# Kernel tuning notes

Measured on AMD Instinct MI355X. Metric: run time of the kernel, lower is better.

The kernel has to match this reference:

```python
import jax, jax.numpy as jnp
import numpy as np

EPS = 1e-6          # module eps for denominator
KERNEL_EPS = 1e-4   # performer softmax_kernel numerical eps


def softmax_kernel(data, projection):
    # data: [n, l, h, e]; projection: [m, e] -> features [n, l, h, m]
    d = data.shape[-1]
    m = projection.shape[0]
    data_normalizer = d ** -0.25
    ratio = m ** -0.5
    data_dash = jnp.einsum('nlhe,me->nlhm', data * data_normalizer, projection)
    diag_data = (0.5 * (data_normalizer ** 2)) * jnp.sum(data * data, axis=-1, keepdims=True)
    # numerically stable exp with per-row max subtraction
    data_dash = ratio * (jnp.exp(data_dash - diag_data - jnp.max(data_dash, axis=-1, keepdims=True)) + KERNEL_EPS)
    return data_dash


def _gaussian_orthogonal_random_matrix(nb_rows, nb_cols, seed=0):
    rng = np.random.default_rng(seed)
    blocks = []
    for _ in range(int(np.ceil(nb_rows / nb_cols))):
        q, _ = np.linalg.qr(rng.standard_normal((nb_cols, nb_cols)))
        blocks.append(q.T)
    proj = np.concatenate(blocks, axis=0)[:nb_rows]
    # scaling=0: chi-distributed row multipliers
    multiplier = np.linalg.norm(rng.standard_normal((nb_rows, nb_cols)), axis=1)
    return (multiplier[:, None] * proj).astype(np.float32)


def setup_inputs() -> dict:
    n, l, h, e = 2, 2048, 8, 64
    nb_features = l  # module: nb_features = l when l >= e
    key = jax.random.key(0)
    kq, kk, kv = jax.random.split(key, 3)
    queries = jax.random.normal(kq, (n, l, h, e), jnp.float32)
    keys = jax.random.normal(kk, (n, l, h, e), jnp.float32)
    values = jax.random.normal(kv, (n, l, h, e), jnp.float32)
    projection = jnp.asarray(_gaussian_orthogonal_random_matrix(nb_features, e))
    return {"queries": queries, "keys": keys, "values": values, "projection": projection}


def reference(queries, keys, values, projection):
    # Performer linear attention, batched (bi=None) branch
    q = softmax_kernel(queries, projection)   # [n, l, h, m]
    k = softmax_kernel(keys, projection)      # [n, l, h, m]
    kv = jnp.einsum('nshm,nshe->nhem', k, values)              # [n, h, e, m]
    z = 1.0 / (jnp.einsum('nlhm,nhm->nlh', q, k.sum(axis=1)) + EPS)  # [n, l, h]
    v = jnp.einsum('nlhm,nhem,nlh->nlhe', q, kv, z)             # [n, l, h, e]
    return v
```

## Files before the change

### kernel.cpp

```cpp
#include <hip/hip_runtime.h>


#define LL 2048
#define HH 8
#define MM 2048
#define ROWSTR 512

#define NORMC 0.35355339059327373f
#define RATIO 0.022097086912079608f
#define KEPS 1e-4f
#define REPS (RATIO * KEPS)
#define EPSD 1e-6f

#define KVSPLIT 2097152
#define RSPLIT 32768

typedef __attribute__((ext_vector_type(8))) short short8;
typedef __attribute__((ext_vector_type(16))) float f32x16;

#define MFMA32(a, b, c) __builtin_amdgcn_mfma_f32_32x32x16_bf16((a), (b), (c), 0, 0, 0)

__device__ __forceinline__ f32x16 zero16() {
    f32x16 v;
    #pragma unroll
    for (int i = 0; i < 16; ++i) v[i] = 0.f;
    return v;
}
__device__ __forceinline__ unsigned short f2bf(float f) {
    union { float f; unsigned int u; } v; v.f = f;
    unsigned int r = v.u + 0x7fffu + ((v.u >> 16) & 1u);
    return (unsigned short)(r >> 16);
}
__device__ __forceinline__ unsigned int pk2(float lo, float hi) {
    return __builtin_amdgcn_perm(__float_as_uint(hi), __float_as_uint(lo), 0x07060302u);
}
__device__ __forceinline__ float bf2f(unsigned short u) {
    union { unsigned int ui; float f; } v; v.ui = ((unsigned int)u) << 16; return v.f;
}

template <bool BF16>
__device__ __forceinline__ void tile_load(const void* src, size_t base, size_t rstride,
                                          int t, uint4& A, uint4& B) {
    const int row = t >> 2, c16 = (t & 3) * 16;
    if (BF16) {
        const unsigned short* p = (const unsigned short*)src + base + (size_t)row * rstride + c16;
        A = *(const uint4*)p;
        B = *(const uint4*)(p + 8);
    } else {
        const float* p = (const float*)src + base + (size_t)row * rstride + c16;
        float4 f0 = ((const float4*)p)[0], f1 = ((const float4*)p)[1];
        float4 f2 = ((const float4*)p)[2], f3 = ((const float4*)p)[3];
        A.x = pk2(f0.x, f0.y); A.y = pk2(f0.z, f0.w);
        A.z = pk2(f1.x, f1.y); A.w = pk2(f1.z, f1.w);
        B.x = pk2(f2.x, f2.y); B.y = pk2(f2.z, f2.w);
        B.z = pk2(f3.x, f3.y); B.w = pk2(f3.z, f3.w);
    }
}
__device__ __forceinline__ void tile_store72(unsigned short* D, int t, uint4 A, uint4 B) {
    const int row = t >> 2, c16 = (t & 3) * 16;
    *(uint4*)&D[row * 72 + c16] = A;
    *(uint4*)&D[row * 72 + c16 + 8] = B;
}

template <bool BF16>
__device__ __forceinline__ void vt_load(const void* V, size_t base, int t, uint4& A, uint4& B) {
    const int s0 = (t & 31) * 2, e0 = (t >> 5) * 8;
    if (BF16) {
        const unsigned short* p = (const unsigned short*)V + base + (size_t)s0 * ROWSTR + e0;
        A = *(const uint4*)p;
        B = *(const uint4*)(p + ROWSTR);
    } else {
        const float* p = (const float*)V + base + (size_t)s0 * ROWSTR + e0;
        float4 f0 = ((const float4*)p)[0], f1 = ((const float4*)p)[1];
        const float* q = p + ROWSTR;
        float4 g0 = ((const float4*)q)[0], g1 = ((const float4*)q)[1];
        A.x = pk2(f0.x, f0.y); A.y = pk2(f0.z, f0.w);
        A.z = pk2(f1.x, f1.y); A.w = pk2(f1.z, f1.w);
        B.x = pk2(g0.x, g0.y); B.y = pk2(g0.z, g0.w);
        B.z = pk2(g1.x, g1.y); B.w = pk2(g1.z, g1.w);
    }
}
__device__ __forceinline__ void vt_store72(unsigned short* VT, int t, uint4 A, uint4 B) {
    const int s0 = (t & 31) * 2, e0 = (t >> 5) * 8;
    const unsigned ua[4] = {A.x, A.y, A.z, A.w}, ub[4] = {B.x, B.y, B.z, B.w};
    #pragma unroll
    for (int i = 0; i < 4; ++i) {
        *(unsigned*)&VT[(e0 + 2 * i) * 72 + s0] = (ua[i] & 0xFFFFu) | (ub[i] << 16);
        *(unsigned*)&VT[(e0 + 2 * i + 1) * 72 + s0] = (ua[i] >> 16) | (ub[i] & 0xFFFF0000u);
    }
}

__device__ __forceinline__ short8 xfrag(const unsigned int pd[8], int cp, int hi) {
    const unsigned int s0 = hi ? pd[4 * cp + 0] : pd[4 * cp + 2];
    const unsigned int s1 = hi ? pd[4 * cp + 1] : pd[4 * cp + 3];
    const unsigned int r0 = (unsigned int)__shfl_xor((int)s0, 32);
    const unsigned int r1 = (unsigned int)__shfl_xor((int)s1, 32);
    union { unsigned int u[4]; short8 s; } v;
    v.u[0] = hi ? r0 : pd[4 * cp + 0];
    v.u[1] = hi ? r1 : pd[4 * cp + 1];
    v.u[2] = hi ? pd[4 * cp + 2] : r0;
    v.u[3] = hi ? pd[4 * cp + 3] : r1;
    return v.s;
}

__global__ void LinearAttention_15985868276494_detect(const unsigned short* __restrict__ P,
                                                      float* __restrict__ flag) {
    if (threadIdx.x == 0) {
        int sane = 1;
        #pragma unroll
        for (int i = 0; i < 16; ++i) {
            const unsigned e = (P[2 * i] >> 7) & 0xFF;
            if (e < 101 || e > 141) sane = 0;
        }
        *flag = sane ? 1.0f : 0.0f;
    }
}

template <bool BF16>
__device__ void stats_impl(const void* X, const void* P, float* cws,
                           unsigned short* Xs, unsigned short* Ps, float* red) {
    const int t = threadIdx.x;
    const int w = t >> 6, ln = t & 31, hi = (t >> 5) & 1;
    const int row_base = blockIdx.x * 128;

    uint4 a0, b0, a1, b1;
    tile_load<BF16>(X, (size_t)row_base * 64, 64, t, a0, b0);
    tile_store72(Xs, t, a0, b0);
    tile_load<BF16>(X, (size_t)(row_base + 64) * 64, 64, t, a1, b1);
    tile_store72(Xs + 64 * 72, t, a1, b1);
    tile_load<BF16>(P, 0, 64, t, a0, b0);
    tile_store72(Ps, t, a0, b0);
    tile_load<BF16>(P, (size_t)64 * 64, 64, t, a1, b1);
    tile_store72(Ps + 64 * 72, t, a1, b1);
    uint4 pA0, pB0, pA1, pB1;
    tile_load<BF16>(P, (size_t)128 * 64, 64, t, pA0, pB0);
    tile_load<BF16>(P, (size_t)192 * 64, 64, t, pA1, pB1);
    __syncthreads();

    short8 xb[4][4];
    #pragma unroll
    for (int xs = 0; xs < 4; ++xs)
        #pragma unroll
        for (int c = 0; c < 4; ++c)
            xb[xs][c] = *(const short8*)&Xs[(32 * xs + ln) * 72 + 16 * c + 8 * hi];

    float rmax4[4] = {-3e38f, -3e38f, -3e38f, -3e38f};
    for (int mt = 0; mt < 16; ++mt) {
        const int cur = mt & 1;
        unsigned short* Pc = Ps + cur * (128 * 72);
        if (mt + 1 < 16) {
            unsigned short* Pn = Ps + (cur ^ 1) * (128 * 72);
            tile_store72(Pn, t, pA0, pB0);
            tile_store72(Pn + 64 * 72, t, pA1, pB1);
            if (mt + 2 < 16) {
                tile_load<BF16>(P, (size_t)((mt + 2) * 128) * 64, 64, t, pA0, pB0);
                tile_load<BF16>(P, (size_t)((mt + 2) * 128 + 64) * 64, 64, t, pA1, pB1);
            }
        }
        #pragma unroll
        for (int xs = 0; xs < 4; ++xs) {
            f32x16 acc = zero16();
            #pragma unroll
            for (int c = 0; c < 4; ++c) {
                const short8 af = *(const short8*)&Pc[(32 * w + ln) * 72 + 16 * c + 8 * hi];
                acc = MFMA32(af, xb[xs][c], acc);
            }
            float m = acc[0];
            #pragma unroll
            for (int r = 1; r < 16; ++r) m = fmaxf(m, acc[r]);
            rmax4[xs] = fmaxf(rmax4[xs], m);
        }
        __syncthreads();
    }
    #pragma unroll
    for (int xs = 0; xs < 4; ++xs) {
        const float m = fmaxf(rmax4[xs], __shfl_xor(rmax4[xs], 32));
        if (hi == 0) red[w * 128 + xs * 32 + ln] = m;
    }
    __syncthreads();
    if (t < 128) {
        const float rm = fmaxf(fmaxf(red[t], red[128 + t]), fmaxf(red[256 + t], red[384 + t]));
        float s2 = 0.f;
        #pragma unroll
        for (int c = 0; c < 64; c += 8) {
            uint4 u = *(const uint4*)&Xs[t * 72 + c];
            const unsigned int ua[4] = {u.x, u.y, u.z, u.w};
            #pragma unroll
            for (int i = 0; i < 4; ++i) {
                const float lo = bf2f((unsigned short)(ua[i] & 0xFFFF));
                const float hv = bf2f((unsigned short)(ua[i] >> 16));
                s2 = fmaf(lo, lo, s2); s2 = fmaf(hv, hv, s2);
            }
        }
        const int rg = row_base + t;
        const int n = rg >> 14, l = (rg >> 3) & 2047, h = rg & 7;
        cws[(size_t)((n << 3) | h) * LL + l] = NORMC * rm + (0.5f * NORMC * NORMC) * s2;
    }
}

__global__ __launch_bounds__(256, 2) void LinearAttention_15985868276494_stats(
        const void* K, const void* Q, const void* P, const float* flag,
        float* c_k, float* c_q) {
    __shared__ unsigned short Xs[128 * 72];
    __shared__ unsigned short Ps[2 * 128 * 72];
    __shared__ float red[512];
    const void* X = (blockIdx.y == 0) ? K : Q;
    float* cws = (blockIdx.y == 0) ? c_k : c_q;
    if (*flag != 0.f) stats_impl<true>(X, P, cws, Xs, Ps, red);
    else stats_impl<false>(X, P, cws, Xs, Ps, red);
}

template <bool BF16>
__device__ void kv_impl(const void* K, const void* V, const void* P, const float* cws,
                        float* kvf01, float* ksum01, char* smem) {
    unsigned short* Ks = (unsigned short*)smem;
    unsigned short* VT = (unsigned short*)(smem + 18432);
    unsigned short* Ps = (unsigned short*)(smem + 36864);
    float* cks = (float*)(smem + 46080);
    float* fin = (float*)smem;

    const int t = threadIdx.x;
    const int w = t >> 6, ln = t & 31, hi = (t >> 5) & 1;
    const int sstrip = w & 1, mstrip = w >> 1;
    const int mt = blockIdx.x, nh = blockIdx.y, sp = blockIdx.z;
    const int n = nh >> 3, h = nh & 7;
    const size_t xbase = (size_t)n * (LL * ROWSTR) + (size_t)h * 64;
    const int st0 = sp * 16;

    {
        uint4 pa, pbv;
        tile_load<BF16>(P, (size_t)(mt * 64) * 64, 64, t, pa, pbv);
        tile_store72(Ps, t, pa, pbv);
    }
    uint4 kA, kB, vA, vB; float ckr = 0.f;
    tile_load<BF16>(K, xbase + (size_t)(st0 * 64) * ROWSTR, ROWSTR, t, kA, kB);
    vt_load<BF16>(V, xbase + (size_t)(st0 * 64) * ROWSTR, t, vA, vB);
    if (t < 64) ckr = cws[(size_t)nh * LL + st0 * 64 + t];
    tile_store72(Ks, t, kA, kB);
    vt_store72(VT, t, vA, vB);
    if (t < 64) cks[t] = ckr;
    tile_load<BF16>(K, xbase + (size_t)((st0 + 1) * 64) * ROWSTR, ROWSTR, t, kA, kB);
    vt_load<BF16>(V, xbase + (size_t)((st0 + 1) * 64) * ROWSTR, t, vA, vB);
    if (t < 64) ckr = cws[(size_t)nh * LL + (st0 + 1) * 64 + t];
    __syncthreads();

    short8 pb[4];
    #pragma unroll
    for (int c = 0; c < 4; ++c)
        pb[c] = *(const short8*)&Ps[(32 * mstrip + ln) * 72 + 16 * c + 8 * hi];
    const short8 ones = {0x3F80, 0x3F80, 0x3F80, 0x3F80, 0x3F80, 0x3F80, 0x3F80, 0x3F80};

    f32x16 akv0 = zero16(), akv1 = zero16(), aks = zero16();

    for (int i = 0; i < 16; ++i) {
        const int cur = i & 1;
        unsigned short* Kc = Ks + cur * 4608;
        unsigned short* Vc = VT + cur * 4608;
        const float* cc = cks + cur * 64;
        if (i + 1 < 16) {
            tile_store72(Ks + (cur ^ 1) * 4608, t, kA, kB);
            vt_store72(VT + (cur ^ 1) * 4608, t, vA, vB);
            if (t < 64) cks[(cur ^ 1) * 64 + t] = ckr;
            if (i + 2 < 16) {
                const int st = st0 + i + 2;
                tile_load<BF16>(K, xbase + (size_t)(st * 64) * ROWSTR, ROWSTR, t, kA, kB);
                vt_load<BF16>(V, xbase + (size_t)(st * 64) * ROWSTR, t, vA, vB);
                if (t < 64) ckr = cws[(size_t)nh * LL + st * 64 + t];
            }
        }
        f32x16 D = zero16();
        #pragma unroll
        for (int c = 0; c < 4; ++c) {
            const short8 af = *(const short8*)&Kc[(32 * sstrip + ln) * 72 + 16 * c + 8 * hi];
            D = MFMA32(af, pb[c], D);
        }
        unsigned int pd[8];
        #pragma unroll
        for (int g = 0; g < 4; ++g) {
            const float4 c4 = *(const float4*)&cc[32 * sstrip + 8 * g + 4 * hi];
            const float ca[4] = {c4.x, c4.y, c4.z, c4.w};
            float f[4];
            #pragma unroll
            for (int b = 0; b < 4; ++b) {
                const float arg = fminf(fmaf(D[4 * g + b], NORMC, -ca[b]), 0.f);
                f[b] = fmaf(__expf(arg), RATIO, REPS);
            }
            pd[2 * g] = pk2(f[0], f[1]);
            pd[2 * g + 1] = pk2(f[2], f[3]);
        }
        #pragma unroll
        for (int cp = 0; cp < 2; ++cp) {
            const short8 bf = xfrag(pd, cp, hi);
            const int scol = 32 * sstrip + 16 * cp + 8 * hi;
            const short8 v0 = *(const short8*)&Vc[ln * 72 + scol];
            const short8 v1 = *(const short8*)&Vc[(32 + ln) * 72 + scol];
            akv0 = MFMA32(v0, bf, akv0);
            akv1 = MFMA32(v1, bf, akv1);
            aks = MFMA32(ones, bf, aks);
        }
        __syncthreads();
    }
    {
        const int slot = (w * 64 + (t & 63)) * 36;
        #pragma unroll
        for (int r = 0; r < 16; ++r) fin[slot + r] = akv0[r];
        #pragma unroll
        for (int r = 0; r < 16; ++r) fin[slot + 16 + r] = akv1[r];
        fin[slot + 32] = aks[0];
    }
    __syncthreads();
    {
        const int e = t >> 2;
        const int t16 = e >> 5, e5 = e & 31;
        const int hi_s = (e5 >> 2) & 1;
        const int reg = 16 * t16 + (e5 & 3) + 4 * (e5 >> 3);
        float* dst = kvf01 + (size_t)sp * KVSPLIT + (size_t)nh * (64 * MM)
                   + (size_t)e * MM + mt * 64 + (t & 3) * 16;
        #pragma unroll
        for (int jq = 0; jq < 4; ++jq) {
            float o[4];
            #pragma unroll
            for (int b = 0; b < 4; ++b) {
                const int m_local = (t & 3) * 16 + 4 * jq + b;
                const int ms = m_local >> 5;
                const int lane_s = hi_s * 32 + (m_local & 31);
                o[b] = fin[((2 * ms) * 64 + lane_s) * 36 + reg]
                     + fin[((2 * ms + 1) * 64 + lane_s) * 36 + reg];
            }
            *(float4*)&dst[4 * jq] = make_float4(o[0], o[1], o[2], o[3]);
        }
        if (t < 64) {
            const int ms = t >> 5;
            const float val = fin[((2 * ms) * 64 + (t & 31)) * 36 + 32]
                            + fin[((2 * ms + 1) * 64 + (t & 31)) * 36 + 32];
            ksum01[(size_t)sp * RSPLIT + (size_t)nh * MM + mt * 64 + t] = val;
        }
    }
}

__global__ __launch_bounds__(256, 3) void LinearAttention_15985868276494_kv(
        const void* K, const void* V, const void* P, const float* flag,
        const float* cws, float* kvf01, float* ksum01) {
    extern __shared__ char smem_kv[];
    if (*flag != 0.f) kv_impl<true>(K, V, P, cws, kvf01, ksum01, smem_kv);
    else kv_impl<false>(K, V, P, cws, kvf01, ksum01, smem_kv);
}

__global__ __launch_bounds__(256) void LinearAttention_15985868276494_reduce(
        const float* __restrict__ kvf01, const float* __restrict__ ksum01,
        unsigned short* __restrict__ kvT, float* __restrict__ ksumW) {
    const int gid = blockIdx.x * 256 + threadIdx.x;
    const size_t i4 = (size_t)gid * 4;
    const float4 a = *(const float4*)&kvf01[i4];
    const float4 b = *(const float4*)&kvf01[KVSPLIT + i4];
    uint2 o;
    o.x = (unsigned)f2bf(a.x + b.x) | ((unsigned)f2bf(a.y + b.y) << 16);
    o.y = (unsigned)f2bf(a.z + b.z) | ((unsigned)f2bf(a.w + b.w) << 16);
    *(uint2*)&kvT[i4] = o;
    if (blockIdx.x < 32) {
        const float4 c = *(const float4*)&ksum01[i4];
        const float4 d = *(const float4*)&ksum01[RSPLIT + i4];
        *(float4*)&ksumW[i4] = make_float4(c.x + d.x, c.y + d.y, c.z + d.z, c.w + d.w);
    }
}

template <bool BF16>
__device__ void out_impl(const void* Q, const void* P, const float* cqw,
                         const unsigned short* kvT, const float* ksum, void* outp,
                         char* smem) {
    unsigned short* Qs = (unsigned short*)smem;
    unsigned short* Ps = (unsigned short*)(smem + 9216);
    unsigned short* KVs = (unsigned short*)(smem + 27648);
    unsigned short* kss = (unsigned short*)(smem + 46080);
    float* fin = (float*)(smem + 9216);

    const int t = threadIdx.x;
    const int w = t >> 6, ln = t & 31, hi = (t >> 5) & 1;
    const int mstrip = w & 1, lstrip = w >> 1;
    const int lb = blockIdx.x, nh = blockIdx.y;
    const int n = nh >> 3, h = nh & 7;
    const size_t qbase = (size_t)n * (LL * ROWSTR) + (size_t)h * 64 + (size_t)(lb * 64) * ROWSTR;
    const size_t kvbase = (size_t)nh * (size_t)(64 * MM);

    {
        uint4 qa, qbv;
        tile_load<BF16>(Q, qbase, ROWSTR, t, qa, qbv);
        tile_store72(Qs, t, qa, qbv);
    }
    uint4 pA, pB, kA, kB; float ksr = 0.f;
    tile_load<BF16>(P, 0, 64, t, pA, pB);
    tile_load<true>(kvT, kvbase, MM, t, kA, kB);
    if (t < 64) ksr = ksum[(size_t)nh * MM + t];
    tile_store72(Ps, t, pA, pB);
    tile_store72(KVs, t, kA, kB);
    if (t < 64) kss[t] = f2bf(ksr);
    tile_load<BF16>(P, (size_t)64 * 64, 64, t, pA, pB);
    tile_load<true>(kvT, kvbase + 64, MM, t, kA, kB);
    if (t < 64) ksr = ksum[(size_t)nh * MM + 64 + t];
    __syncthreads();

    short8 qb[4];
    #pragma unroll
    for (int c = 0; c < 4; ++c)
        qb[c] = *(const short8*)&Qs[(32 * lstrip + ln) * 72 + 16 * c + 8 * hi];
    const float cq = cqw[(size_t)nh * LL + lb * 64 + lstrip * 32 + ln];

    f32x16 ao0 = zero16(), ao1 = zero16(), ad = zero16();

    for (int mt = 0; mt < 32; ++mt) {
        const int cur = mt & 1;
        unsigned short* Pc = Ps + cur * 4608;
        unsigned short* Kc = KVs + cur * 4608;
        const unsigned short* ksc = kss + cur * 64;
        if (mt + 1 < 32) {
            tile_store72(Ps + (cur ^ 1) * 4608, t, pA, pB);
            tile_store72(KVs + (cur ^ 1) * 4608, t, kA, kB);
            if (t < 64) kss[(cur ^ 1) * 64 + t] = f2bf(ksr);
            if (mt + 2 < 32) {
                tile_load<BF16>(P, (size_t)((mt + 2) * 64) * 64, 64, t, pA, pB);
                tile_load<true>(kvT, kvbase + (mt + 2) * 64, MM, t, kA, kB);
                if (t < 64) ksr = ksum[(size_t)nh * MM + (mt + 2) * 64 + t];
            }
        }
        f32x16 D = zero16();
        #pragma unroll
        for (int c = 0; c < 4; ++c) {
            const short8 af = *(const short8*)&Pc[(32 * mstrip + ln) * 72 + 16 * c + 8 * hi];
            D = MFMA32(af, qb[c], D);
        }
        unsigned int pd[8];
        #pragma unroll
        for (int g = 0; g < 4; ++g) {
            float f[4];
            #pragma unroll
            for (int b = 0; b < 4; ++b) {
                const float arg = fminf(fmaf(D[4 * g + b], NORMC, -cq), 0.f);
                f[b] = fmaf(__expf(arg), RATIO, REPS);
            }
            pd[2 * g] = pk2(f[0], f[1]);
            pd[2 * g + 1] = pk2(f[2], f[3]);
        }
        #pragma unroll
        for (int cp = 0; cp < 2; ++cp) {
            const short8 bf = xfrag(pd, cp, hi);
            const int mcol = 32 * mstrip + 16 * cp + 8 * hi;
            const short8 a0 = *(const short8*)&Kc[ln * 72 + mcol];
            const short8 a1 = *(const short8*)&Kc[(32 + ln) * 72 + mcol];
            const short8 k8 = *(const short8*)&ksc[mcol];
            ao0 = MFMA32(a0, bf, ao0);
            ao1 = MFMA32(a1, bf, ao1);
            ad = MFMA32(k8, bf, ad);
        }
        __syncthreads();
    }
    {
        const int slot = (w * 64 + (t & 63)) * 36;
        #pragma unroll
        for (int r = 0; r < 16; ++r) fin[slot + r] = ao0[r];
        #pragma unroll
        for (int r = 0; r < 16; ++r) fin[slot + 16 + r] = ao1[r];
        fin[slot + 32] = ad[0];
    }
    __syncthreads();
    {
        const int l_local = t >> 2, eg = t & 3;
        const int ls = l_local >> 5, lane_l = l_local & 31;
        const float adt = fin[((2 * ls) * 64 + lane_l) * 36 + 32]
                        + fin[((2 * ls + 1) * 64 + lane_l) * 36 + 32];
        const float z = 1.0f / (adt + EPSD);
        const int l = lb * 64 + l_local;
        const size_t rowoff = ((size_t)(n * LL + l) * HH + h) * 64 + eg * 16;
        float vals[16];
        #pragma unroll
        for (int j = 0; j < 16; ++j) {
            const int e = eg * 16 + j;
            const int t16 = e >> 5, e5 = e & 31;
            const int hi_s = (e5 >> 2) & 1;
            const int reg = 16 * t16 + (e5 & 3) + 4 * (e5 >> 3);
            const int lane_s = hi_s * 32 + lane_l;
            vals[j] = (fin[((2 * ls) * 64 + lane_s) * 36 + reg]
                     + fin[((2 * ls + 1) * 64 + lane_s) * 36 + reg]) * z;
        }
        if (BF16) {
            uint4 o0, o1;
            o0.x = (unsigned)f2bf(vals[0]) | ((unsigned)f2bf(vals[1]) << 16);
            o0.y = (unsigned)f2bf(vals[2]) | ((unsigned)f2bf(vals[3]) << 16);
            o0.z = (unsigned)f2bf(vals[4]) | ((unsigned)f2bf(vals[5]) << 16);
            o0.w = (unsigned)f2bf(vals[6]) | ((unsigned)f2bf(vals[7]) << 16);
            o1.x = (unsigned)f2bf(vals[8]) | ((unsigned)f2bf(vals[9]) << 16);
            o1.y = (unsigned)f2bf(vals[10]) | ((unsigned)f2bf(vals[11]) << 16);
            o1.z = (unsigned)f2bf(vals[12]) | ((unsigned)f2bf(vals[13]) << 16);
            o1.w = (unsigned)f2bf(vals[14]) | ((unsigned)f2bf(vals[15]) << 16);
            unsigned short* op = (unsigned short*)outp + rowoff;
            *(uint4*)op = o0;
            *(uint4*)(op + 8) = o1;
        } else {
            float* op = (float*)outp + rowoff;
            #pragma unroll
            for (int q4 = 0; q4 < 4; ++q4)
                *(float4*)&op[4 * q4] = make_float4(vals[4 * q4], vals[4 * q4 + 1],
                                                    vals[4 * q4 + 2], vals[4 * q4 + 3]);
        }
    }
}

__global__ __launch_bounds__(256, 3) void LinearAttention_15985868276494_out(
        const void* Q, const void* P, const float* flag, const float* cqw,
        const unsigned short* kvT, const float* ksum, void* outp) {
    extern __shared__ char smem_out[];
    if (*flag != 0.f) out_impl<true>(Q, P, cqw, kvT, ksum, outp, smem_out);
    else out_impl<false>(Q, P, cqw, kvT, ksum, outp, smem_out);
}

extern "C" void kernel_launch(void* const* d_in, const int* in_sizes, int n_in,
                              void* d_out, int out_size, void* d_ws, size_t ws_size,
                              hipStream_t stream) {
    const void* Q = d_in[0];
    const void* K = d_in[1];
    const void* V = d_in[2];
    const void* P = d_in[3];

    float* W = (float*)d_ws;
    float* flag = W;
    float* c_k = W + 16;
    float* c_q = c_k + 32768;
    float* ksum01 = c_q + 32768;
    float* kvf01 = ksum01 + 2 * RSPLIT;
    float* ksumW = kvf01 + 2 * KVSPLIT;
    unsigned short* kvTW = (unsigned short*)(ksumW + RSPLIT);

    LinearAttention_15985868276494_detect<<<1, 64, 0, stream>>>(
        (const unsigned short*)P, flag);
    LinearAttention_15985868276494_stats<<<dim3(256, 2), 256, 0, stream>>>(
        K, Q, P, flag, c_k, c_q);
    LinearAttention_15985868276494_kv<<<dim3(32, 16, 2), 256, 46592, stream>>>(
        K, V, P, flag, c_k, kvf01, ksum01);
    LinearAttention_15985868276494_reduce<<<2048, 256, 0, stream>>>(
        kvf01, ksum01, kvTW, ksumW);
    LinearAttention_15985868276494_out<<<dim3(32, 16), 256, 46592, stream>>>(
        Q, P, flag, c_q, kvTW, ksumW, d_out);
}
```

Measured before the change: 192.3 us.

## Split out kernel over m, shrink LDS, use exp2 and smaller stats tiles

```diff
diff --git a/kernel.cpp b/kernel.cpp
--- a/kernel.cpp
+++ b/kernel.cpp
@@ -7,6 +7,8 @@
 #define ROWSTR 512
 
 #define NORMC 0.35355339059327373f
+#define LOG2E 1.4426950408889634f
+#define NORMC2 (NORMC * LOG2E)
 #define RATIO 0.022097086912079608f
 #define KEPS 1e-4f
 #define REPS (RATIO * KEPS)
@@ -121,65 +123,48 @@
                            unsigned short* Xs, unsigned short* Ps, float* red) {
     const int t = threadIdx.x;
     const int w = t >> 6, ln = t & 31, hi = (t >> 5) & 1;
-    const int row_base = blockIdx.x * 128;
-
-    uint4 a0, b0, a1, b1;
+    const int rstrip = w & 1, mstrip = w >> 1;
+    const int row_base = blockIdx.x * 64;
+
+    uint4 a0, b0;
     tile_load<BF16>(X, (size_t)row_base * 64, 64, t, a0, b0);
     tile_store72(Xs, t, a0, b0);
-    tile_load<BF16>(X, (size_t)(row_base + 64) * 64, 64, t, a1, b1);
-    tile_store72(Xs + 64 * 72, t, a1, b1);
     tile_load<BF16>(P, 0, 64, t, a0, b0);
     tile_store72(Ps, t, a0, b0);
-    tile_load<BF16>(P, (size_t)64 * 64, 64, t, a1, b1);
-    tile_store72(Ps + 64 * 72, t, a1, b1);
-    uint4 pA0, pB0, pA1, pB1;
-    tile_load<BF16>(P, (size_t)128 * 64, 64, t, pA0, pB0);
-    tile_load<BF16>(P, (size_t)192 * 64, 64, t, pA1, pB1);
-    __syncthreads();
-
-    short8 xb[4][4];
+    uint4 pA, pB;
+    tile_load<BF16>(P, (size_t)64 * 64, 64, t, pA, pB);
+    __syncthreads();
+
+    short8 xb[4];
     #pragma unroll
-    for (int xs = 0; xs < 4; ++xs)
-        #pragma unroll
-        for (int c = 0; c < 4; ++c)
-            xb[xs][c] = *(const short8*)&Xs[(32 * xs + ln) * 72 + 16 * c + 8 * hi];
-
-    float rmax4[4] = {-3e38f, -3e38f, -3e38f, -3e38f};
-    for (int mt = 0; mt < 16; ++mt) {
-        const int cur = mt & 1;
-        unsigned short* Pc = Ps + cur * (128 * 72);
-        if (mt + 1 < 16) {
-            unsigned short* Pn = Ps + (cur ^ 1) * (128 * 72);
-            tile_store72(Pn, t, pA0, pB0);
-            tile_store72(Pn + 64 * 72, t, pA1, pB1);
-            if (mt + 2 < 16) {
-                tile_load<BF16>(P, (size_t)((mt + 2) * 128) * 64, 64, t, pA0, pB0);
-                tile_load<BF16>(P, (size_t)((mt + 2) * 128 + 64) * 64, 64, t, pA1, pB1);
-            }
-        }
-        #pragma unroll
-        for (int xs = 0; xs < 4; ++xs) {
-            f32x16 acc = zero16();
-            #pragma unroll
-            for (int c = 0; c < 4; ++c) {
-                const short8 af = *(const short8*)&Pc[(32 * w + ln) * 72 + 16 * c + 8 * hi];
-                acc = MFMA32(af, xb[xs][c], acc);
-            }
-            float m = acc[0];
-            #pragma unroll
-            for (int r = 1; r < 16; ++r) m = fmaxf(m, acc[r]);
-            rmax4[xs] = fmaxf(rmax4[xs], m);
-        }
+    for (int c = 0; c < 4; ++c)
+        xb[c] = *(const short8*)&Xs[(32 * rstrip + ln) * 72 + 16 * c + 8 * hi];
+
+    float rmax = -3e38f;
+    for (int i = 0; i < 32; ++i) {
+        const int cur = i & 1;
+        unsigned short* Pc = Ps + cur * 4608;
+        if (i + 1 < 32) {
+            tile_store72(Ps + (cur ^ 1) * 4608, t, pA, pB);
+            if (i + 2 < 32)
+                tile_load<BF16>(P, (size_t)((i + 2) * 64) * 64, 64, t, pA, pB);
+        }
+        f32x16 acc = zero16();
+        #pragma unroll
+        for (int c = 0; c < 4; ++c) {
+            const short8 af = *(const short8*)&Pc[(32 * mstrip + ln) * 72 + 16 * c + 8 * hi];
+            acc = MFMA32(af, xb[c], acc);
+        }
+        #pragma unroll
+        for (int r = 0; r < 16; ++r) rmax = fmaxf(rmax, acc[r]);
         __syncthreads();
     }
-    #pragma unroll
-    for (int xs = 0; xs < 4; ++xs) {
-        const float m = fmaxf(rmax4[xs], __shfl_xor(rmax4[xs], 32));
-        if (hi == 0) red[w * 128 + xs * 32 + ln] = m;
-    }
-    __syncthreads();
-    if (t < 128) {
-        const float rm = fmaxf(fmaxf(red[t], red[128 + t]), fmaxf(red[256 + t], red[384 + t]));
+    rmax = fmaxf(rmax, __shfl_xor(rmax, 32));
+    if (hi == 0) red[w * 32 + ln] = rmax;
+    __syncthreads();
+    if (t < 64) {
+        const int rs = t >> 5;
+        const float rm = fmaxf(red[rs * 32 + (t & 31)], red[(rs + 2) * 32 + (t & 31)]);
         float s2 = 0.f;
         #pragma unroll
         for (int c = 0; c < 64; c += 8) {
@@ -194,16 +179,17 @@
         }
         const int rg = row_base + t;
         const int n = rg >> 14, l = (rg >> 3) & 2047, h = rg & 7;
-        cws[(size_t)((n << 3) | h) * LL + l] = NORMC * rm + (0.5f * NORMC * NORMC) * s2;
-    }
-}
-
-__global__ __launch_bounds__(256, 2) void LinearAttention_15985868276494_stats(
+        cws[(size_t)((n << 3) | h) * LL + l] =
+            (NORMC * rm + (0.5f * NORMC * NORMC) * s2) * LOG2E;
+    }
+}
+
+__global__ __launch_bounds__(256, 4) void LinearAttention_15985868276494_stats(
         const void* K, const void* Q, const void* P, const float* flag,
         float* c_k, float* c_q) {
-    __shared__ unsigned short Xs[128 * 72];
-    __shared__ unsigned short Ps[2 * 128 * 72];
-    __shared__ float red[512];
+    __shared__ unsigned short Xs[64 * 72];
+    __shared__ unsigned short Ps[2 * 64 * 72];
+    __shared__ float red[128];
     const void* X = (blockIdx.y == 0) ? K : Q;
     float* cws = (blockIdx.y == 0) ? c_k : c_q;
     if (*flag != 0.f) stats_impl<true>(X, P, cws, Xs, Ps, red);
@@ -215,8 +201,7 @@
                         float* kvf01, float* ksum01, char* smem) {
     unsigned short* Ks = (unsigned short*)smem;
     unsigned short* VT = (unsigned short*)(smem + 18432);
-    unsigned short* Ps = (unsigned short*)(smem + 36864);
-    float* cks = (float*)(smem + 46080);
+    float* cks = (float*)(smem + 36864);
     float* fin = (float*)smem;
 
     const int t = threadIdx.x;
@@ -227,6 +212,7 @@
     const size_t xbase = (size_t)n * (LL * ROWSTR) + (size_t)h * 64;
     const int st0 = sp * 16;
 
+    unsigned short* Ps = Ks + 4608;
     {
         uint4 pa, pbv;
         tile_load<BF16>(P, (size_t)(mt * 64) * 64, 64, t, pa, pbv);
@@ -248,6 +234,7 @@
     #pragma unroll
     for (int c = 0; c < 4; ++c)
         pb[c] = *(const short8*)&Ps[(32 * mstrip + ln) * 72 + 16 * c + 8 * hi];
+    __syncthreads();
     const short8 ones = {0x3F80, 0x3F80, 0x3F80, 0x3F80, 0x3F80, 0x3F80, 0x3F80, 0x3F80};
 
     f32x16 akv0 = zero16(), akv1 = zero16(), aks = zero16();
@@ -282,8 +269,8 @@
             float f[4];
             #pragma unroll
             for (int b = 0; b < 4; ++b) {
-                const float arg = fminf(fmaf(D[4 * g + b], NORMC, -ca[b]), 0.f);
-                f[b] = fmaf(__expf(arg), RATIO, REPS);
+                const float arg = fminf(fmaf(D[4 * g + b], NORMC2, -ca[b]), 0.f);
+                f[b] = fmaf(__builtin_amdgcn_exp2f(arg), RATIO, REPS);
             }
             pd[2 * g] = pk2(f[0], f[1]);
             pd[2 * g + 1] = pk2(f[2], f[3]);
@@ -301,7 +288,7 @@
         __syncthreads();
     }
     {
-        const int slot = (w * 64 + (t & 63)) * 36;
+        const int slot = (w * 64 + (t & 63)) * 33;
         #pragma unroll
         for (int r = 0; r < 16; ++r) fin[slot + r] = akv0[r];
         #pragma unroll
@@ -324,21 +311,21 @@
                 const int m_local = (t & 3) * 16 + 4 * jq + b;
                 const int ms = m_local >> 5;
                 const int lane_s = hi_s * 32 + (m_local & 31);
-                o[b] = fin[((2 * ms) * 64 + lane_s) * 36 + reg]
-                     + fin[((2 * ms + 1) * 64 + lane_s) * 36 + reg];
+                o[b] = fin[((2 * ms) * 64 + lane_s) * 33 + reg]
+                     + fin[((2 * ms + 1) * 64 + lane_s) * 33 + reg];
             }
             *(float4*)&dst[4 * jq] = make_float4(o[0], o[1], o[2], o[3]);
         }
         if (t < 64) {
             const int ms = t >> 5;
-            const float val = fin[((2 * ms) * 64 + (t & 31)) * 36 + 32]
-                            + fin[((2 * ms + 1) * 64 + (t & 31)) * 36 + 32];
+            const float val = fin[((2 * ms) * 64 + (t & 31)) * 33 + 32]
+                            + fin[((2 * ms + 1) * 64 + (t & 31)) * 33 + 32];
             ksum01[(size_t)sp * RSPLIT + (size_t)nh * MM + mt * 64 + t] = val;
         }
     }
 }
 
-__global__ __launch_bounds__(256, 3) void LinearAttention_15985868276494_kv(
+__global__ __launch_bounds__(256, 4) void LinearAttention_15985868276494_kv(
         const void* K, const void* V, const void* P, const float* flag,
         const float* cws, float* kvf01, float* ksum01) {
     extern __shared__ char smem_kv[];
@@ -366,37 +353,38 @@
 
 template <bool BF16>
 __device__ void out_impl(const void* Q, const void* P, const float* cqw,
-                         const unsigned short* kvT, const float* ksum, void* outp,
-                         char* smem) {
-    unsigned short* Qs = (unsigned short*)smem;
-    unsigned short* Ps = (unsigned short*)(smem + 9216);
-    unsigned short* KVs = (unsigned short*)(smem + 27648);
-    unsigned short* kss = (unsigned short*)(smem + 46080);
-    float* fin = (float*)(smem + 9216);
+                         const unsigned short* kvT, const float* ksum,
+                         float* po, float* pad, char* smem) {
+    unsigned short* Ps = (unsigned short*)smem;
+    unsigned short* KVs = (unsigned short*)(smem + 18432);
+    unsigned short* kss = (unsigned short*)(smem + 36864);
+    float* fin = (float*)smem;
 
     const int t = threadIdx.x;
     const int w = t >> 6, ln = t & 31, hi = (t >> 5) & 1;
     const int mstrip = w & 1, lstrip = w >> 1;
-    const int lb = blockIdx.x, nh = blockIdx.y;
+    const int lb = blockIdx.x, nh = blockIdx.y, sp = blockIdx.z;
     const int n = nh >> 3, h = nh & 7;
     const size_t qbase = (size_t)n * (LL * ROWSTR) + (size_t)h * 64 + (size_t)(lb * 64) * ROWSTR;
     const size_t kvbase = (size_t)nh * (size_t)(64 * MM);
-
+    const int mt0 = sp * 16;
+
+    unsigned short* Qs = Ps + 4608;
     {
         uint4 qa, qbv;
         tile_load<BF16>(Q, qbase, ROWSTR, t, qa, qbv);
         tile_store72(Qs, t, qa, qbv);
     }
     uint4 pA, pB, kA, kB; float ksr = 0.f;
-    tile_load<BF16>(P, 0, 64, t, pA, pB);
-    tile_load<true>(kvT, kvbase, MM, t, kA, kB);
-    if (t < 64) ksr = ksum[(size_t)nh * MM + t];
+    tile_load<BF16>(P, (size_t)(mt0 * 64) * 64, 64, t, pA, pB);
+    tile_load<true>(kvT, kvbase + mt0 * 64, MM, t, kA, kB);
+    if (t < 64) ksr = ksum[(size_t)nh * MM + mt0 * 64 + t];
     tile_store72(Ps, t, pA, pB);
     tile_store72(KVs, t, kA, kB);
     if (t < 64) kss[t] = f2bf(ksr);
-    tile_load<BF16>(P, (size_t)64 * 64, 64, t, pA, pB);
-    tile_load<true>(kvT, kvbase + 64, MM, t, kA, kB);
-    if (t < 64) ksr = ksum[(size_t)nh * MM + 64 + t];
+    tile_load<BF16>(P, (size_t)((mt0 + 1) * 64) * 64, 64, t, pA, pB);
+    tile_load<true>(kvT, kvbase + (mt0 + 1) * 64, MM, t, kA, kB);
+    if (t < 64) ksr = ksum[(size_t)nh * MM + (mt0 + 1) * 64 + t];
     __syncthreads();
 
     short8 qb[4];
@@ -404,22 +392,23 @@
     for (int c = 0; c < 4; ++c)
         qb[c] = *(const short8*)&Qs[(32 * lstrip + ln) * 72 + 16 * c + 8 * hi];
     const float cq = cqw[(size_t)nh * LL + lb * 64 + lstrip * 32 + ln];
+    __syncthreads();
 
     f32x16 ao0 = zero16(), ao1 = zero16(), ad = zero16();
 
-    for (int mt = 0; mt < 32; ++mt) {
-        const int cur = mt & 1;
+    for (int i = 0; i < 16; ++i) {
+        const int cur = i & 1;
         unsigned short* Pc = Ps + cur * 4608;
         unsigned short* Kc = KVs + cur * 4608;
         const unsigned short* ksc = kss + cur * 64;
-        if (mt + 1 < 32) {
+        if (i + 1 < 16) {
             tile_store72(Ps + (cur ^ 1) * 4608, t, pA, pB);
             tile_store72(KVs + (cur ^ 1) * 4608, t, kA, kB);
             if (t < 64) kss[(cur ^ 1) * 64 + t] = f2bf(ksr);
-            if (mt + 2 < 32) {
-                tile_load<BF16>(P, (size_t)((mt + 2) * 64) * 64, 64, t, pA, pB);
-                tile_load<true>(kvT, kvbase + (mt + 2) * 64, MM, t, kA, kB);
-                if (t < 64) ksr = ksum[(size_t)nh * MM + (mt + 2) * 64 + t];
+            if (i + 2 < 16) {
+                tile_load<BF16>(P, (size_t)((mt0 + i + 2) * 64) * 64, 64, t, pA, pB);
+                tile_load<true>(kvT, kvbase + (mt0 + i + 2) * 64, MM, t, kA, kB);
+                if (t < 64) ksr = ksum[(size_t)nh * MM + (mt0 + i + 2) * 64 + t];
             }
         }
         f32x16 D = zero16();
@@ -434,8 +423,8 @@
             float f[4];
             #pragma unroll
             for (int b = 0; b < 4; ++b) {
-                const float arg = fminf(fmaf(D[4 * g + b], NORMC, -cq), 0.f);
-                f[b] = fmaf(__expf(arg), RATIO, REPS);
+                const float arg = fminf(fmaf(D[4 * g + b], NORMC2, -cq), 0.f);
+                f[b] = fmaf(__builtin_amdgcn_exp2f(arg), RATIO, REPS);
             }
             pd[2 * g] = pk2(f[0], f[1]);
             pd[2 * g + 1] = pk2(f[2], f[3]);
@@ -454,7 +443,7 @@
         __syncthreads();
     }
     {
-        const int slot = (w * 64 + (t & 63)) * 36;
+        const int slot = (w * 64 + (t & 63)) * 33;
         #pragma unroll
         for (int r = 0; r < 16; ++r) fin[slot + r] = ao0[r];
         #pragma unroll
@@ -465,51 +454,76 @@
     {
         const int l_local = t >> 2, eg = t & 3;
         const int ls = l_local >> 5, lane_l = l_local & 31;
-        const float adt = fin[((2 * ls) * 64 + lane_l) * 36 + 32]
-                        + fin[((2 * ls + 1) * 64 + lane_l) * 36 + 32];
-        const float z = 1.0f / (adt + EPSD);
+        const float adt = fin[((2 * ls) * 64 + lane_l) * 33 + 32]
+                        + fin[((2 * ls + 1) * 64 + lane_l) * 33 + 32];
         const int l = lb * 64 + l_local;
-        const size_t rowoff = ((size_t)(n * LL + l) * HH + h) * 64 + eg * 16;
-        float vals[16];
-        #pragma unroll
-        for (int j = 0; j < 16; ++j) {
-            const int e = eg * 16 + j;
-            const int t16 = e >> 5, e5 = e & 31;
-            const int hi_s = (e5 >> 2) & 1;
-            const int reg = 16 * t16 + (e5 & 3) + 4 * (e5 >> 3);
-            const int lane_s = hi_s * 32 + lane_l;
-            vals[j] = (fin[((2 * ls) * 64 + lane_s) * 36 + reg]
-                     + fin[((2 * ls + 1) * 64 + lane_s) * 36 + reg]) * z;
-        }
-        if (BF16) {
-            uint4 o0, o1;
-            o0.x = (unsigned)f2bf(vals[0]) | ((unsigned)f2bf(vals[1]) << 16);
-            o0.y = (unsigned)f2bf(vals[2]) | ((unsigned)f2bf(vals[3]) << 16);
-            o0.z = (unsigned)f2bf(vals[4]) | ((unsigned)f2bf(vals[5]) << 16);
-            o0.w = (unsigned)f2bf(vals[6]) | ((unsigned)f2bf(vals[7]) << 16);
-            o1.x = (unsigned)f2bf(vals[8]) | ((unsigned)f2bf(vals[9]) << 16);
-            o1.y = (unsigned)f2bf(vals[10]) | ((unsigned)f2bf(vals[11]) << 16);
-            o1.z = (unsigned)f2bf(vals[12]) | ((unsigned)f2bf(vals[13]) << 16);
-            o1.w = (unsigned)f2bf(vals[14]) | ((unsigned)f2bf(vals[15]) << 16);
-            unsigned short* op = (unsigned short*)outp + rowoff;
-            *(uint4*)op = o0;
-            *(uint4*)(op + 8) = o1;
-        } else {
-            float* op = (float*)outp + rowoff;
+        const size_t row = (size_t)(n * LL + l) * HH + h;
+        if (eg == 0) pad[(size_t)sp * RSPLIT + row] = adt;
+        float* dst = po + (size_t)sp * KVSPLIT + row * 64 + eg * 16;
+        #pragma unroll
+        for (int jq = 0; jq < 4; ++jq) {
+            float o[4];
             #pragma unroll
-            for (int q4 = 0; q4 < 4; ++q4)
-                *(float4*)&op[4 * q4] = make_float4(vals[4 * q4], vals[4 * q4 + 1],
-                                                    vals[4 * q4 + 2], vals[4 * q4 + 3]);
-        }
-    }
-}
-
-__global__ __launch_bounds__(256, 3) void LinearAttention_15985868276494_out(
+            for (int b = 0; b < 4; ++b) {
+                const int e = eg * 16 + 4 * jq + b;
+                const int t16 = e >> 5, e5 = e & 31;
+                const int hi_s = (e5 >> 2) & 1;
+                const int reg = 16 * t16 + (e5 & 3) + 4 * (e5 >> 3);
+                const int lane_s = hi_s * 32 + lane_l;
+                o[b] = fin[((2 * ls) * 64 + lane_s) * 33 + reg]
+                     + fin[((2 * ls + 1) * 64 + lane_s) * 33 + reg];
+            }
+            *(float4*)&dst[4 * jq] = make_float4(o[0], o[1], o[2], o[3]);
+        }
+    }
+}
+
+__global__ __launch_bounds__(256, 4) void LinearAttention_15985868276494_out(
         const void* Q, const void* P, const float* flag, const float* cqw,
-        const unsigned short* kvT, const float* ksum, void* outp) {
+        const unsigned short* kvT, const float* ksum, float* po, float* pad) {
     extern __shared__ char smem_out[];
-    if (*flag != 0.f) out_impl<true>(Q, P, cqw, kvT, ksum, outp, smem_out);
-    else out_impl<false>(Q, P, cqw, kvT, ksum, outp, smem_out);
+    if (*flag != 0.f) out_impl<true>(Q, P, cqw, kvT, ksum, po, pad, smem_out);
+    else out_impl<false>(Q, P, cqw, kvT, ksum, po, pad, smem_out);
+}
+
+__global__ __launch_bounds__(256) void LinearAttention_15985868276494_out2(
+        const float* __restrict__ po, const float* __restrict__ pad,
+        const float* __restrict__ flag, void* __restrict__ outp) {
+    const int gid = blockIdx.x * 256 + threadIdx.x;
+    const int row = gid >> 2, eg = gid & 3;
+    const float adt = pad[row] + pad[RSPLIT + row];
+    const float z = 1.0f / (adt + EPSD);
+    const size_t base = (size_t)row * 64 + eg * 16;
+    float vals[16];
+    #pragma unroll
+    for (int q4 = 0; q4 < 4; ++q4) {
+        const float4 a = *(const float4*)&po[base + 4 * q4];
+        const float4 b = *(const float4*)&po[KVSPLIT + base + 4 * q4];
+        vals[4 * q4 + 0] = (a.x + b.x) * z;
+        vals[4 * q4 + 1] = (a.y + b.y) * z;
+        vals[4 * q4 + 2] = (a.z + b.z) * z;
+        vals[4 * q4 + 3] = (a.w + b.w) * z;
+    }
+    if (*flag != 0.f) {
+        uint4 o0, o1;
+        o0.x = (unsigned)f2bf(vals[0]) | ((unsigned)f2bf(vals[1]) << 16);
+        o0.y = (unsigned)f2bf(vals[2]) | ((unsigned)f2bf(vals[3]) << 16);
+        o0.z = (unsigned)f2bf(vals[4]) | ((unsigned)f2bf(vals[5]) << 16);
+        o0.w = (unsigned)f2bf(vals[6]) | ((unsigned)f2bf(vals[7]) << 16);
+        o1.x = (unsigned)f2bf(vals[8]) | ((unsigned)f2bf(vals[9]) << 16);
+        o1.y = (unsigned)f2bf(vals[10]) | ((unsigned)f2bf(vals[11]) << 16);
+        o1.z = (unsigned)f2bf(vals[12]) | ((unsigned)f2bf(vals[13]) << 16);
+        o1.w = (unsigned)f2bf(vals[14]) | ((unsigned)f2bf(vals[15]) << 16);
+        unsigned short* op = (unsigned short*)outp + base;
+        *(uint4*)op = o0;
+        *(uint4*)(op + 8) = o1;
+    } else {
+        float* op = (float*)outp + base;
+        #pragma unroll
+        for (int q4 = 0; q4 < 4; ++q4)
+            *(float4*)&op[4 * q4] = make_float4(vals[4 * q4], vals[4 * q4 + 1],
+                                                vals[4 * q4 + 2], vals[4 * q4 + 3]);
+    }
 }
 
 extern "C" void kernel_launch(void* const* d_in, const int* in_sizes, int n_in,
@@ -531,12 +545,14 @@
 
     LinearAttention_15985868276494_detect<<<1, 64, 0, stream>>>(
         (const unsigned short*)P, flag);
-    LinearAttention_15985868276494_stats<<<dim3(256, 2), 256, 0, stream>>>(
+    LinearAttention_15985868276494_stats<<<dim3(512, 2), 256, 0, stream>>>(
         K, Q, P, flag, c_k, c_q);
-    LinearAttention_15985868276494_kv<<<dim3(32, 16, 2), 256, 46592, stream>>>(
+    LinearAttention_15985868276494_kv<<<dim3(32, 16, 2), 256, 37376, stream>>>(
         K, V, P, flag, c_k, kvf01, ksum01);
     LinearAttention_15985868276494_reduce<<<2048, 256, 0, stream>>>(
         kvf01, ksum01, kvTW, ksumW);
-    LinearAttention_15985868276494_out<<<dim3(32, 16), 256, 46592, stream>>>(
-        Q, P, flag, c_q, kvTW, ksumW, d_out);
-}
+    LinearAttention_15985868276494_out<<<dim3(32, 16, 2), 256, 37120, stream>>>(
+        Q, P, flag, c_q, kvTW, ksumW, kvf01, ksum01);
+    LinearAttention_15985868276494_out2<<<512, 256, 0, stream>>>(
+        kvf01, ksum01, flag, d_out);
+}
```

Result: slower. 215.1 us (+11.9%).
